# Optimization experiments

Measured on AMD Instinct MI355X. Metric: run time of the kernel, lower is better.

The kernel has to match this reference:

```python
import jax, jax.numpy as jnp
import numpy as np

B, S, K, H = 512, 128, 4, 128  # batch, seq_len, interest_num, hidden_size
ROUTING_TIMES = 3
EPS = 1e-9


def setup_inputs() -> dict:
    key = jax.random.key(0)
    k1, k2 = jax.random.split(key)
    item_eb = jax.random.normal(k1, (B, S, H), dtype=jnp.float32)
    mask = jnp.ones((B, S), dtype=jnp.float32)
    # learned bilinear map parameter (bilinear_type == 2)
    w = jax.random.normal(k2, (1, S, K * H, H), dtype=jnp.float32) * 0.02
    return {"item_eb": item_eb, "mask": mask, "w": w}


def _squash(cap):
    # cap: [B, K, 1, H]
    n = jnp.sum(cap * cap, axis=-1, keepdims=True)
    return (n / (1.0 + n) / jnp.sqrt(n + EPS)) * cap


def reference(item_eb, mask, w):
    # bilinear_type==2: sum(w[:, :S] * item_eb[:, :, None, :], axis=3)
    # expressed as an einsum to avoid the [B,S,K*H,H] intermediate
    item_eb_hat = jnp.einsum('bsh,sdh->bsd', item_eb, w[0])          # [B, S, K*H]
    item_eb_hat = item_eb_hat.reshape(B, S, K, H).transpose(0, 2, 1, 3)  # [B, K, S, H]
    hat_iter = jax.lax.stop_gradient(item_eb_hat)  # stop_grad=True

    atten_mask = jnp.broadcast_to(mask[:, None, :], (B, K, S))
    capsule_weight = jnp.zeros((B, K, S), dtype=item_eb.dtype)  # bilinear_type > 0

    interest_capsule = None
    for i in range(ROUTING_TIMES):
        # torch F.softmax with implicit dim on a 3D tensor -> dim=0 (legacy)
        sw = jax.nn.softmax(capsule_weight, axis=0)
        sw = jnp.where(atten_mask == 0, 0.0, sw)[:, :, None, :]  # [B, K, 1, S]
        src = hat_iter if i < 2 else item_eb_hat
        interest_capsule = _squash(jnp.matmul(sw, src))  # [B, K, 1, H]
        if i < 2:
            delta = jnp.matmul(hat_iter, interest_capsule.transpose(0, 1, 3, 2))  # [B,K,S,1]
            capsule_weight = capsule_weight + delta.reshape(B, K, S)

    return interest_capsule.reshape(B, K, H)
```

## Files before the change

### kernel.cpp

```cpp
#include <hip/hip_runtime.h>
#include <math.h>

#define BB 512
#define SS 128
#define KK 4
#define HH 128
#define DD 512

typedef __attribute__((ext_vector_type(8))) short bf16x8;
typedef __attribute__((ext_vector_type(4))) float f32x4;

__device__ __forceinline__ unsigned short f2bf(float f) {
  unsigned u = __float_as_uint(f);
  unsigned r = u + 0x7fffu + ((u >> 16) & 1u);
  return (unsigned short)(r >> 16);
}
__device__ __forceinline__ float bfhi(unsigned u) { return __uint_as_float(u & 0xffff0000u); }
__device__ __forceinline__ float bflo(unsigned u) { return __uint_as_float(u << 16); }

__device__ __forceinline__ void async_cp16(const void* g, void* l) {
  __builtin_amdgcn_global_load_lds(
      (const __attribute__((address_space(1))) unsigned int*)g,
      (__attribute__((address_space(3))) unsigned int*)l, 16, 0, 0);
}

__global__ __launch_bounds__(256) void einsum_mfma(
    const float* __restrict__ item,
    const float* __restrict__ w,
    unsigned short* __restrict__ hat)
{
  __shared__ unsigned short Al[128 * 64];
  __shared__ unsigned short Wl[128 * 64];
  const int s  = blockIdx.x;
  const int b0 = (blockIdx.y & 3) * 128;
  const int dt = blockIdx.y >> 2;
  const int d0 = dt * 128;
  const int t  = threadIdx.x;
  const int lane = t & 63, wv = t >> 6;
  const int qm = wv & 1, qn = wv >> 1;
  const int n16 = lane & 15, kq = lane >> 4;
  const int cj = t & 15, r0 = t >> 4;

  const float* Abase = item + ((size_t)b0 * SS + s) * HH;
  const float* Wbase = w + ((size_t)s * DD + d0) * HH;

  f32x4 acc[4][4] = {};
  #pragma unroll
  for (int ks = 0; ks < 128; ks += 64) {
    if (ks) __syncthreads();
    #pragma unroll
    for (int j = 0; j < 8; j++) {
      const int r = r0 + 16 * j;
      float4 va = *(const float4*)(Abase + (size_t)r * (SS * HH) + ks + cj * 4);
      float4 vw = *(const float4*)(Wbase + (size_t)r * HH + ks + cj * 4);
      ushort4 oa, ow;
      oa.x = f2bf(va.x); oa.y = f2bf(va.y); oa.z = f2bf(va.z); oa.w = f2bf(va.w);
      ow.x = f2bf(vw.x); ow.y = f2bf(vw.y); ow.z = f2bf(vw.z); ow.w = f2bf(vw.w);
      const int goff = (((cj >> 1) + r) & 7) * 8 + (cj & 1) * 4;
      *(ushort4*)&Al[r * 64 + goff] = oa;
      *(ushort4*)&Wl[r * 64 + goff] = ow;
    }
    __syncthreads();
    #pragma unroll
    for (int kk = 0; kk < 2; kk++) {
      bf16x8 af[4], bfr[4];
      #pragma unroll
      for (int i = 0; i < 4; i++) {
        const int ra = qm * 64 + i * 16 + n16;
        const int rb = qn * 64 + i * 16 + n16;
        af[i]  = *(const bf16x8*)&Wl[ra * 64 + ((kk * 4 + kq + ra) & 7) * 8];
        bfr[i] = *(const bf16x8*)&Al[rb * 64 + ((kk * 4 + kq + rb) & 7) * 8];
      }
      #pragma unroll
      for (int i = 0; i < 4; i++)
        #pragma unroll
        for (int j = 0; j < 4; j++)
          acc[i][j] = __builtin_amdgcn_mfma_f32_16x16x32_bf16(af[i], bfr[j], acc[i][j], 0, 0, 0);
    }
  }

  const int sx = s & 15;
  #pragma unroll
  for (int j = 0; j < 4; j++) {
    const int b = b0 + qn * 64 + j * 16 + n16;
    char* orow = (char*)(hat + (((size_t)b * KK + dt) * SS + s) * HH);
    #pragma unroll
    for (int i = 0; i < 4; i++) {
      const int h = qm * 64 + i * 16 + kq * 4;
      ushort4 o;
      o.x = f2bf(acc[i][j][0]); o.y = f2bf(acc[i][j][1]);
      o.z = f2bf(acc[i][j][2]); o.w = f2bf(acc[i][j][3]);
      *(ushort4*)(orow + ((((h >> 3) ^ sx) << 4) | ((h & 4) << 1))) = o;
    }
  }
}

__global__ __launch_bounds__(256) void softmax_k(
    const float* __restrict__ cw, const float* __restrict__ mask,
    float* __restrict__ sw)
{
  __shared__ float rbuf[4];
  const int s = blockIdx.x, k = blockIdx.y, t = threadIdx.x;
  const size_t base = ((size_t)k * SS + s) * BB;
  float v0 = cw[base + t], v1 = cw[base + 256 + t];
  float m = fmaxf(v0, v1);
  #pragma unroll
  for (int o = 32; o; o >>= 1) m = fmaxf(m, __shfl_xor(m, o));
  if ((t & 63) == 0) rbuf[t >> 6] = m;
  __syncthreads();
  m = fmaxf(fmaxf(rbuf[0], rbuf[1]), fmaxf(rbuf[2], rbuf[3]));
  float e0 = expf(v0 - m), e1 = expf(v1 - m);
  float ssum = e0 + e1;
  #pragma unroll
  for (int o = 32; o; o >>= 1) ssum += __shfl_xor(ssum, o);
  __syncthreads();
  if ((t & 63) == 0) rbuf[t >> 6] = ssum;
  __syncthreads();
  float inv = 1.f / (rbuf[0] + rbuf[1] + rbuf[2] + rbuf[3]);
  float m0 = mask[(size_t)t * SS + s];
  float m1 = mask[(size_t)(t + 256) * SS + s];
  sw[base + t]       = (m0 == 0.f) ? 0.f : e0 * inv;
  sw[base + 256 + t] = (m1 == 0.f) ? 0.f : e1 * inv;
}

__global__ __launch_bounds__(256) void routing_k(
    const unsigned short* __restrict__ hat, const float* __restrict__ mask,
    const float* __restrict__ sw_in, float* __restrict__ cw,
    float* __restrict__ out, int mode)
{
  __shared__ unsigned short hat_l[128 * 128];
  __shared__ float sw_l[128];
  __shared__ float4 red4[8][32];
  __shared__ float4 cq4[32];
  const int b = blockIdx.x, k = blockIdx.y, t = threadIdx.x;
  const int wv = t >> 6;

  const char* slab = (const char*)(hat + ((size_t)b * KK + k) * SS * HH);
  #pragma unroll
  for (int j = 0; j < 8; j++)
    async_cp16(slab + j * 4096 + t * 16,
               (char*)hat_l + j * 4096 + wv * 1024);

  if (t < 128) {
    sw_l[t] = (mode == 0)
      ? ((mask[(size_t)b * SS + t] == 0.f) ? 0.f : (1.f / 512.f))
      : sw_in[((size_t)k * SS + t) * BB + b];
  }
  __syncthreads();

  {
    const int h4 = t & 31, sg = t >> 5;
    const char* base = (const char*)hat_l;
    float4 a = make_float4(0.f, 0.f, 0.f, 0.f);
    #pragma unroll 4
    for (int i = 0; i < 16; i++) {
      const int s = sg * 16 + i;
      uint2 v = *(const uint2*)(base + s * 256 +
                 ((((h4 >> 1) ^ (s & 15)) << 4) | ((h4 & 1) << 3)));
      float wv2 = sw_l[s];
      a.x = fmaf(wv2, bflo(v.x), a.x);
      a.y = fmaf(wv2, bfhi(v.x), a.y);
      a.z = fmaf(wv2, bflo(v.y), a.z);
      a.w = fmaf(wv2, bfhi(v.y), a.w);
    }
    red4[sg][h4] = a;
  }
  __syncthreads();

  if (t < 32) {
    float4 cap = red4[0][t];
    #pragma unroll
    for (int sg = 1; sg < 8; sg++) {
      float4 r = red4[sg][t];
      cap.x += r.x; cap.y += r.y; cap.z += r.z; cap.w += r.w;
    }
    float sq = cap.x * cap.x + cap.y * cap.y + cap.z * cap.z + cap.w * cap.w;
    #pragma unroll
    for (int o = 16; o; o >>= 1) sq += __shfl_xor(sq, o);
    const float n = sq;
    const float fac = n / (1.f + n) / sqrtf(n + 1e-9f);
    cap.x *= fac; cap.y *= fac; cap.z *= fac; cap.w *= fac;
    cq4[t] = cap;
    if (mode == 2)
      ((float4*)(out + ((size_t)b * KK + k) * HH))[t] = cap;
  }
  __syncthreads();

  if (mode < 2) {
    const int s = t >> 1, hh = t & 1;
    const char* rowp = (const char*)hat_l + s * 256;
    const int sx = s & 15;
    float d = 0.f;
    #pragma unroll
    for (int j = 0; j < 8; j++) {
      uint4 v = *(const uint4*)(rowp + (((hh * 8 + j) ^ sx) << 4));
      float4 qa = cq4[hh * 16 + 2 * j];
      float4 qb = cq4[hh * 16 + 2 * j + 1];
      d += bflo(v.x) * qa.x + bfhi(v.x) * qa.y
         + bflo(v.y) * qa.z + bfhi(v.y) * qa.w
         + bflo(v.z) * qb.x + bfhi(v.z) * qb.y
         + bflo(v.w) * qb.z + bfhi(v.w) * qb.w;
    }
    d += __shfl_xor(d, 1);
    if (hh == 0) {
      float* p = cw + ((size_t)k * SS + s) * BB + b;
      if (mode == 0) *p = d; else *p += d;
    }
  }
}

extern "C" void kernel_launch(void* const* d_in, const int* in_sizes, int n_in,
                              void* d_out, int out_size, void* d_ws, size_t ws_size,
                              hipStream_t stream) {
  const float* item_eb = (const float*)d_in[0];
  const float* mask    = (const float*)d_in[1];
  const float* w       = (const float*)d_in[2];
  float* out = (float*)d_out;

  char* ws = (char*)d_ws;
  unsigned short* hat_bf = (unsigned short*)ws;
  float* cw  = (float*)(ws + 67108864);
  float* swb = (float*)(ws + 68157440);

  einsum_mfma<<<dim3(128, 16), 256, 0, stream>>>(item_eb, w, hat_bf);

  routing_k<<<dim3(BB, KK), 256, 0, stream>>>(hat_bf, mask, nullptr, cw, out, 0);
  softmax_k<<<dim3(SS, KK), 256, 0, stream>>>(cw, mask, swb);
  routing_k<<<dim3(BB, KK), 256, 0, stream>>>(hat_bf, mask, swb, cw, out, 1);
  softmax_k<<<dim3(SS, KK), 256, 0, stream>>>(cw, mask, swb);
  routing_k<<<dim3(BB, KK), 256, 0, stream>>>(hat_bf, mask, swb, cw, out, 2);
}
```

Measured before the change: 174.4 us.

## Reuse item tile across all d-tiles with double-buffered W prefetch in einsum

The einsum kernel now loads the full 128x128 item tile once per block and loops over all four d-tiles, streaming W through a double-buffered LDS slab with register prefetch. This cuts redundant item loads and conversions and overlaps W global loads with MFMA work, but the grid shrinks to 512 blocks and register pressure rises. The routing kernel also replaces the block-wide barrier after async copies with per-wave loads and a waitcnt, and skips a barrier in mode 2.

```diff
diff --git a/kernel.cpp b/kernel.cpp
--- a/kernel.cpp
+++ b/kernel.cpp
@@ -15,6 +15,10 @@
   unsigned r = u + 0x7fffu + ((u >> 16) & 1u);
   return (unsigned short)(r >> 16);
 }
+__device__ __forceinline__ ushort4 f2bf4(float4 v) {
+  ushort4 o; o.x = f2bf(v.x); o.y = f2bf(v.y); o.z = f2bf(v.z); o.w = f2bf(v.w);
+  return o;
+}
 __device__ __forceinline__ float bfhi(unsigned u) { return __uint_as_float(u & 0xffff0000u); }
 __device__ __forceinline__ float bflo(unsigned u) { return __uint_as_float(u << 16); }
 
@@ -29,68 +33,94 @@
     const float* __restrict__ w,
     unsigned short* __restrict__ hat)
 {
-  __shared__ unsigned short Al[128 * 64];
-  __shared__ unsigned short Wl[128 * 64];
+  __shared__ unsigned short Al[128 * 128];
+  __shared__ unsigned short Wl[2][128 * 64];
   const int s  = blockIdx.x;
-  const int b0 = (blockIdx.y & 3) * 128;
-  const int dt = blockIdx.y >> 2;
-  const int d0 = dt * 128;
+  const int b0 = blockIdx.y * 128;
   const int t  = threadIdx.x;
-  const int lane = t & 63, wv = t >> 6;
-  const int qm = wv & 1, qn = wv >> 1;
+  const int lane = t & 63, wvq = t >> 6;
+  const int qm = wvq & 1, qn = wvq >> 1;
   const int n16 = lane & 15, kq = lane >> 4;
-  const int cj = t & 15, r0 = t >> 4;
 
   const float* Abase = item + ((size_t)b0 * SS + s) * HH;
-  const float* Wbase = w + ((size_t)s * DD + d0) * HH;
-
-  f32x4 acc[4][4] = {};
-  #pragma unroll
-  for (int ks = 0; ks < 128; ks += 64) {
-    if (ks) __syncthreads();
-    #pragma unroll
-    for (int j = 0; j < 8; j++) {
-      const int r = r0 + 16 * j;
-      float4 va = *(const float4*)(Abase + (size_t)r * (SS * HH) + ks + cj * 4);
-      float4 vw = *(const float4*)(Wbase + (size_t)r * HH + ks + cj * 4);
-      ushort4 oa, ow;
-      oa.x = f2bf(va.x); oa.y = f2bf(va.y); oa.z = f2bf(va.z); oa.w = f2bf(va.w);
-      ow.x = f2bf(vw.x); ow.y = f2bf(vw.y); ow.z = f2bf(vw.z); ow.w = f2bf(vw.w);
-      const int goff = (((cj >> 1) + r) & 7) * 8 + (cj & 1) * 4;
-      *(ushort4*)&Al[r * 64 + goff] = oa;
-      *(ushort4*)&Wl[r * 64 + goff] = ow;
-    }
-    __syncthreads();
-    #pragma unroll
-    for (int kk = 0; kk < 2; kk++) {
-      bf16x8 af[4], bfr[4];
+  const float* Wbase = w + (size_t)s * DD * HH;
+
+  const int ac = t & 31, ar0 = t >> 5;
+  const int wc = t & 15, wr0 = t >> 4;
+  float4 apre[16];
+  #pragma unroll
+  for (int j = 0; j < 16; ++j)
+    apre[j] = *(const float4*)(Abase + (size_t)(ar0 + 8 * j) * (SS * HH) + ac * 4);
+  float4 wpre[8];
+  #pragma unroll
+  for (int j = 0; j < 8; ++j)
+    wpre[j] = *(const float4*)(Wbase + (size_t)(wr0 + 16 * j) * HH + wc * 4);
+
+  #pragma unroll
+  for (int j = 0; j < 16; ++j) {
+    const int r = ar0 + 8 * j;
+    const int lg = ac >> 1;
+    *(ushort4*)&Al[r * 128 + ((lg ^ (r & 15)) * 8) + (ac & 1) * 4] = f2bf4(apre[j]);
+  }
+  #pragma unroll
+  for (int j = 0; j < 8; ++j) {
+    const int r = wr0 + 16 * j;
+    *(ushort4*)&Wl[0][r * 64 + ((((wc >> 1) + r) & 7) * 8) + (wc & 1) * 4] = f2bf4(wpre[j]);
+  }
+  __syncthreads();
+
+  const int sx = s & 15;
+  int buf = 0;
+  for (int dt = 0; dt < 4; ++dt) {
+    f32x4 acc[4][4] = {};
+    #pragma unroll
+    for (int hs = 0; hs < 2; ++hs) {
+      const int step = dt * 2 + hs;
+      if (step < 7) {
+        const int d0n = ((step + 1) >> 1) * 128;
+        const int ksn = ((step + 1) & 1) * 64;
+        #pragma unroll
+        for (int j = 0; j < 8; ++j)
+          wpre[j] = *(const float4*)(Wbase + (size_t)(d0n + wr0 + 16 * j) * HH + ksn + wc * 4);
+      }
       #pragma unroll
-      for (int i = 0; i < 4; i++) {
-        const int ra = qm * 64 + i * 16 + n16;
-        const int rb = qn * 64 + i * 16 + n16;
-        af[i]  = *(const bf16x8*)&Wl[ra * 64 + ((kk * 4 + kq + ra) & 7) * 8];
-        bfr[i] = *(const bf16x8*)&Al[rb * 64 + ((kk * 4 + kq + rb) & 7) * 8];
-      }
+      for (int kk = 0; kk < 2; ++kk) {
+        bf16x8 af[4], bfr[4];
+        #pragma unroll
+        for (int i = 0; i < 4; ++i) {
+          const int ra = qm * 64 + i * 16 + n16;
+          const int rb = qn * 64 + i * 16 + n16;
+          af[i]  = *(const bf16x8*)&Wl[buf][ra * 64 + ((kk * 4 + kq + ra) & 7) * 8];
+          bfr[i] = *(const bf16x8*)&Al[rb * 128 + (((hs * 8 + kk * 4 + kq) ^ (rb & 15)) * 8)];
+        }
+        #pragma unroll
+        for (int i = 0; i < 4; ++i)
+          #pragma unroll
+          for (int j = 0; j < 4; ++j)
+            acc[i][j] = __builtin_amdgcn_mfma_f32_16x16x32_bf16(af[i], bfr[j], acc[i][j], 0, 0, 0);
+      }
+      if (step < 7) {
+        #pragma unroll
+        for (int j = 0; j < 8; ++j) {
+          const int r = wr0 + 16 * j;
+          *(ushort4*)&Wl[buf ^ 1][r * 64 + ((((wc >> 1) + r) & 7) * 8) + (wc & 1) * 4] = f2bf4(wpre[j]);
+        }
+        __syncthreads();
+        buf ^= 1;
+      }
+    }
+    #pragma unroll
+    for (int j = 0; j < 4; ++j) {
+      const int b = b0 + qn * 64 + j * 16 + n16;
+      char* orow = (char*)(hat + (((size_t)b * KK + dt) * SS + s) * HH);
       #pragma unroll
-      for (int i = 0; i < 4; i++)
-        #pragma unroll
-        for (int j = 0; j < 4; j++)
-          acc[i][j] = __builtin_amdgcn_mfma_f32_16x16x32_bf16(af[i], bfr[j], acc[i][j], 0, 0, 0);
-    }
-  }
-
-  const int sx = s & 15;
-  #pragma unroll
-  for (int j = 0; j < 4; j++) {
-    const int b = b0 + qn * 64 + j * 16 + n16;
-    char* orow = (char*)(hat + (((size_t)b * KK + dt) * SS + s) * HH);
-    #pragma unroll
-    for (int i = 0; i < 4; i++) {
-      const int h = qm * 64 + i * 16 + kq * 4;
-      ushort4 o;
-      o.x = f2bf(acc[i][j][0]); o.y = f2bf(acc[i][j][1]);
-      o.z = f2bf(acc[i][j][2]); o.w = f2bf(acc[i][j][3]);
-      *(ushort4*)(orow + ((((h >> 3) ^ sx) << 4) | ((h & 4) << 1))) = o;
+      for (int i = 0; i < 4; ++i) {
+        const int h = qm * 64 + i * 16 + kq * 4;
+        ushort4 o;
+        o.x = f2bf(acc[i][j][0]); o.y = f2bf(acc[i][j][1]);
+        o.z = f2bf(acc[i][j][2]); o.w = f2bf(acc[i][j][3]);
+        *(ushort4*)(orow + ((((h >> 3) ^ sx) << 4) | ((h & 4) << 1))) = o;
+      }
     }
   }
 }
@@ -133,20 +163,21 @@
   __shared__ float4 red4[8][32];
   __shared__ float4 cq4[32];
   const int b = blockIdx.x, k = blockIdx.y, t = threadIdx.x;
-  const int wv = t >> 6;
-
-  const char* slab = (const char*)(hat + ((size_t)b * KK + k) * SS * HH);
-  #pragma unroll
-  for (int j = 0; j < 8; j++)
-    async_cp16(slab + j * 4096 + t * 16,
-               (char*)hat_l + j * 4096 + wv * 1024);
-
-  if (t < 128) {
-    sw_l[t] = (mode == 0)
-      ? ((mask[(size_t)b * SS + t] == 0.f) ? 0.f : (1.f / 512.f))
-      : sw_in[((size_t)k * SS + t) * BB + b];
-  }
-  __syncthreads();
+  const int wv = t >> 6, lane = t & 63;
+
+  const char* slab = (const char*)(hat + ((size_t)b * KK + k) * SS * HH) + wv * 8192;
+  char* ldst = (char*)hat_l + wv * 8192;
+  #pragma unroll
+  for (int j = 0; j < 8; ++j)
+    async_cp16(slab + j * 1024 + lane * 16, ldst + j * 1024);
+
+  if (lane < 32) {
+    const int sv = wv * 32 + lane;
+    sw_l[sv] = (mode == 0)
+      ? ((mask[(size_t)b * SS + sv] == 0.f) ? 0.f : (1.f / 512.f))
+      : sw_in[((size_t)k * SS + sv) * BB + b];
+  }
+  asm volatile("s_waitcnt vmcnt(0) lgkmcnt(0)" ::: "memory");
 
   {
     const int h4 = t & 31, sg = t >> 5;
@@ -154,10 +185,10 @@
     float4 a = make_float4(0.f, 0.f, 0.f, 0.f);
     #pragma unroll 4
     for (int i = 0; i < 16; i++) {
-      const int s = sg * 16 + i;
-      uint2 v = *(const uint2*)(base + s * 256 +
-                 ((((h4 >> 1) ^ (s & 15)) << 4) | ((h4 & 1) << 3)));
-      float wv2 = sw_l[s];
+      const int sr = sg * 16 + i;
+      uint2 v = *(const uint2*)(base + sr * 256 +
+                 ((((h4 >> 1) ^ (sr & 15)) << 4) | ((h4 & 1) << 3)));
+      float wv2 = sw_l[sr];
       a.x = fmaf(wv2, bflo(v.x), a.x);
       a.y = fmaf(wv2, bfhi(v.x), a.y);
       a.z = fmaf(wv2, bflo(v.y), a.z);
@@ -184,12 +215,12 @@
     if (mode == 2)
       ((float4*)(out + ((size_t)b * KK + k) * HH))[t] = cap;
   }
-  __syncthreads();
 
   if (mode < 2) {
-    const int s = t >> 1, hh = t & 1;
-    const char* rowp = (const char*)hat_l + s * 256;
-    const int sx = s & 15;
+    __syncthreads();
+    const int sr = t >> 1, hh = t & 1;
+    const char* rowp = (const char*)hat_l + sr * 256;
+    const int sx = sr & 15;
     float d = 0.f;
     #pragma unroll
     for (int j = 0; j < 8; j++) {
@@ -203,7 +234,7 @@
     }
     d += __shfl_xor(d, 1);
     if (hh == 0) {
-      float* p = cw + ((size_t)k * SS + s) * BB + b;
+      float* p = cw + ((size_t)k * SS + sr) * BB + b;
       if (mode == 0) *p = d; else *p += d;
     }
   }
@@ -222,7 +253,7 @@
   float* cw  = (float*)(ws + 67108864);
   float* swb = (float*)(ws + 68157440);
 
-  einsum_mfma<<<dim3(128, 16), 256, 0, stream>>>(item_eb, w, hat_bf);
+  einsum_mfma<<<dim3(128, 4), 256, 0, stream>>>(item_eb, w, hat_bf);
 
   routing_k<<<dim3(BB, KK), 256, 0, stream>>>(hat_bf, mask, nullptr, cw, out, 0);
   softmax_k<<<dim3(SS, KK), 256, 0, stream>>>(cw, mask, swb);
```

After: 172.2 us. Within noise of the previous version (-1.3%).
